# Performance work log

Measured on AMD Instinct MI355X. Metric: run time of the kernel, lower is better.

The kernel has to match this reference:

```python
import jax, jax.numpy as jnp
import numpy as np

B, C, HD, NL, NP = 2, 256, 8, 4, 4
D = C // HD
SHAPES = np.array([[128, 128], [64, 64], [32, 32], [16, 16]], dtype=np.int64)
LV = int(SHAPES.prod(axis=1).sum())  # 21760
LQ = LV


def _bilinear(v_l, loc, Hl, Wl):
    # v_l: [B, HD, Nl, D]; loc: [B, Q, HD, P, 2] normalized to [0,1]
    # Matches torch grid_sample(bilinear, padding='zeros', align_corners=False)
    Bq, Q, _, P, _ = loc.shape
    x = loc[..., 0] * Wl - 0.5
    y = loc[..., 1] * Hl - 0.5
    x0f = jnp.floor(x)
    y0f = jnp.floor(y)
    lx, ly = x - x0f, y - y0f
    x0 = x0f.astype(jnp.int32)
    y0 = y0f.astype(jnp.int32)

    def corner(xi, yi, w):
        valid = (xi >= 0) & (xi < Wl) & (yi >= 0) & (yi < Hl)
        idx = jnp.clip(yi, 0, Hl - 1) * Wl + jnp.clip(xi, 0, Wl - 1)  # [B,Q,HD,P]
        idx = idx.transpose(0, 2, 1, 3).reshape(Bq, HD, Q * P)
        g = jnp.take_along_axis(v_l, idx[..., None], axis=2).reshape(Bq, HD, Q, P, D)
        wm = jnp.where(valid, w, 0.0).transpose(0, 2, 1, 3)[..., None]  # [B,HD,Q,P,1]
        return g * wm

    return (corner(x0, y0, (1 - lx) * (1 - ly))
            + corner(x0 + 1, y0, lx * (1 - ly))
            + corner(x0, y0 + 1, (1 - lx) * ly)
            + corner(x0 + 1, y0 + 1, lx * ly))


def _msda(query, reference_points, value, shapes, W_off, b_off, W_attn, b_attn, W_val, b_val, W_out, b_out):
    # value projection -> per-head layout [B, HD, Lv, D]
    v = (value @ W_val + b_val).reshape(B, LV, HD, D).transpose(0, 2, 1, 3)
    off = (query @ W_off + b_off).reshape(B, LQ, HD, NL, NP, 2)
    aw = jax.nn.softmax((query @ W_attn + b_attn).reshape(B, LQ, HD, NL * NP), axis=-1)
    aw = aw.reshape(B, LQ, HD, NL, NP)
    norm = jnp.asarray(shapes[:, ::-1].copy(), query.dtype)  # (W_l, H_l) per level
    # sampling locations: [B, Lq, HD, NL, NP, 2]
    loc = reference_points[:, :, None, :, None, :] + off / norm[None, None, None, :, None, :]
    out = jnp.zeros((B, HD, LQ, D), query.dtype)
    start = 0
    for l in range(NL):  # small static loop over feature levels
        Hl, Wl = int(shapes[l, 0]), int(shapes[l, 1])
        samp = _bilinear(v[:, :, start:start + Hl * Wl], loc[:, :, :, l], Hl, Wl)  # [B,HD,Q,P,D]
        out = out + jnp.einsum('bhqpd,bhqp->bhqd', samp, aw[:, :, :, l].transpose(0, 2, 1, 3))
        start += Hl * Wl
    out = out.transpose(0, 2, 1, 3).reshape(B, LQ, C)
    # output projection + residual (identity = query, dropout inactive at eval)
    return out @ W_out + b_out + query


def setup_inputs():
    key = jax.random.key(0)
    ks = jax.random.split(key, 8)
    sc = 1.0 / np.sqrt(C)
    return {
        "query": jax.random.normal(ks[0], (B, LQ, C), jnp.float32),
        "reference_points": jax.random.uniform(ks[1], (B, LQ, NL, 2), dtype=jnp.float32),
        "value": jax.random.normal(ks[2], (B, LV, C), jnp.float32),
        "spatial_shapes": SHAPES,
        "level_start_index": np.concatenate([[0], np.cumsum(SHAPES.prod(axis=1))[:-1]]).astype(np.int64),
        "W_off": jax.random.normal(ks[3], (C, HD * NL * NP * 2), jnp.float32) * 0.01,
        "b_off": jax.random.normal(ks[4], (HD * NL * NP * 2,), jnp.float32) * 0.01,
        "W_attn": jax.random.normal(ks[5], (C, HD * NL * NP), jnp.float32) * 0.02,
        "b_attn": jnp.zeros((HD * NL * NP,), jnp.float32),
        "W_val": jax.random.normal(ks[6], (C, C), jnp.float32) * sc,
        "b_val": jnp.zeros((C,), jnp.float32),
        "W_out": jax.random.normal(ks[7], (C, C), jnp.float32) * sc,
        "b_out": jnp.zeros((C,), jnp.float32),
    }


def reference(query, reference_points, value, spatial_shapes, level_start_index, W_off, b_off, W_attn, b_attn, W_val, b_val, W_out, b_out):
    shapes = np.asarray(spatial_shapes)  # static level geometry
    del level_start_index  # level offsets derived directly from shapes
    return _msda(query, reference_points, value, shapes, W_off, b_off, W_attn, b_attn, W_val, b_val, W_out, b_out)
```

## Files before the change

### kernel.cpp

```cpp
#include <hip/hip_runtime.h>

#define LQN 21760
#define LVN 21760
#define BATCH 2
#define CDIM 256
#define HDN 8
#define DDIM 32
#define PADCELLS 22736

typedef __attribute__((ext_vector_type(8))) short short8;
typedef __attribute__((ext_vector_type(4))) float f32x4;
typedef __attribute__((ext_vector_type(2))) float f32x2;

__device__ __forceinline__ unsigned short f2bf(float f) {
  union { float f; unsigned int u; } v; v.f = f;
  unsigned int r = v.u + 0x7fffu + ((v.u >> 16) & 1u);
  return (unsigned short)(r >> 16);
}
__device__ __forceinline__ float bflo(unsigned int u) {
  union { unsigned int u; float f; } v; v.u = u << 16; return v.f;
}
__device__ __forceinline__ float bfhi(unsigned int u) {
  union { unsigned int u; float f; } v; v.u = u & 0xffff0000u; return v.f;
}
__device__ __forceinline__ unsigned pk2bf(float lo, float hi) {
  unsigned r;
  asm("v_cvt_pk_bf16_f32 %0, %1, %2" : "=v"(r) : "v"(lo), "v"(hi));
  return r;
}

template <int IMM>
__device__ __forceinline__ float swzf(float v) {
  return __int_as_float(__builtin_amdgcn_ds_swizzle(__float_as_int(v), IMM));
}
template <int IMM>
__device__ __forceinline__ unsigned swzu(unsigned v) {
  return (unsigned)__builtin_amdgcn_ds_swizzle((int)v, IMM);
}

__global__ __launch_bounds__(256) void prep_zero_kernel(
    const float* __restrict__ Wval, const float* __restrict__ Woff,
    const float* __restrict__ Wattn, const float* __restrict__ Wout,
    unsigned short* __restrict__ wtval, unsigned short* __restrict__ wtoa,
    unsigned short* __restrict__ wtout, unsigned short* __restrict__ vbf) {
  const int b = blockIdx.x;
  if (b < 384) {
    const int idx = b * 256 + threadIdx.x;
    const int n = idx >> 8, k = idx & 255;
    if (idx < 65536) {
      wtval[idx] = f2bf(Wval[k * 256 + n]);
      wtout[idx] = f2bf(Wout[k * 256 + n]);
    }
    const float v = (n < 256) ? Woff[k * 256 + n] : Wattn[k * 128 + (n - 256)];
    wtoa[idx] = f2bf(v);
  } else {
    const int b2 = b - 384;
    const int img = b2 >> 4;
    const int tid = (b2 & 15) * 256 + threadIdx.x;
    const int cell = tid >> 2;
    const int chunk = tid & 3;
    if (cell >= 976) return;
    const int lvl = (cell >= 516) + (cell >= 776) + (cell >= 908);
    const int base = (lvl == 0) ? 0 : (lvl == 1) ? 516 : (lvl == 2) ? 776 : 908;
    const int W2 = (lvl == 0) ? 130 : (lvl == 1) ? 66 : (lvl == 2) ? 34 : 18;
    const int pst = (lvl == 0) ? 0 : (lvl == 1) ? 16900 : (lvl == 2) ? 21256 : 22412;
    const int bb = cell - base;
    int x, y;
    if (bb < W2) { y = 0; x = bb; }
    else if (bb < 2 * W2) { y = W2 - 1; x = bb - W2; }
    else { const int r = bb - 2 * W2; y = 1 + (r >> 1); x = (r & 1) ? (W2 - 1) : 0; }
    const size_t off = (((size_t)img * PADCELLS + pst + y * W2 + x) << 5) + chunk * 8;
    *(uint4*)(vbf + off) = (uint4){0u, 0u, 0u, 0u};
  }
}

template <int MODE>
__device__ __forceinline__ void gemm_body(
    unsigned short* lsA0, unsigned short* lsB0, const int bx, const int by,
    const float* __restrict__ Af32, const unsigned short* __restrict__ Abf,
    const unsigned short* __restrict__ Wt, const float* __restrict__ bias0,
    const float* __restrict__ bias1, const float* __restrict__ resid,
    unsigned short* __restrict__ out_bf, float* __restrict__ out_f32) {
  constexpr int K = 256;
  constexpr int LDSS = 40;
  constexpr int LBUF = 128 * LDSS;
  const int m0 = bx * 128;
  const int n0 = by * 128;
  const int t = threadIdx.x;
  const int w = t >> 6;
  const int l = t & 63;
  const int wr = (w >> 1) * 64;
  const int wc = (w & 1) * 64;
  const int fr = l & 15;
  const int kk = (l >> 4) * 8;

  f32x4 acc[4][4];
#pragma unroll
  for (int mi = 0; mi < 4; ++mi)
#pragma unroll
    for (int ci = 0; ci < 4; ++ci) acc[mi][ci] = (f32x4){0.f, 0.f, 0.f, 0.f};

  const int ar8 = t >> 3, ak8 = (t & 7) * 4;
  const int ar4 = t >> 2, ak4 = (t & 3) * 8;

  float4 fa[4];
  uint4 ua2[2];
  uint4 ub[2];

#define LOADA(kt)                                                            \
  do {                                                                       \
    const int k0_ = (kt) * 32;                                               \
    if (MODE == 2) {                                                         \
      ua2[0] = *(const uint4*)(Abf + (size_t)(m0 + ar4) * K + k0_ + ak4);    \
      ua2[1] = *(const uint4*)(Abf + (size_t)(m0 + 64 + ar4) * K + k0_ + ak4);\
    } else {                                                                 \
      fa[0] = *(const float4*)(Af32 + (size_t)(m0 + ar8) * K + k0_ + ak8);   \
      fa[1] = *(const float4*)(Af32 + (size_t)(m0 + 32 + ar8) * K + k0_ + ak8);\
      fa[2] = *(const float4*)(Af32 + (size_t)(m0 + 64 + ar8) * K + k0_ + ak8);\
      fa[3] = *(const float4*)(Af32 + (size_t)(m0 + 96 + ar8) * K + k0_ + ak8);\
    }                                                                        \
    ub[0] = *(const uint4*)(Wt + (size_t)(n0 + ar4) * K + k0_ + ak4);        \
    ub[1] = *(const uint4*)(Wt + (size_t)(n0 + 64 + ar4) * K + k0_ + ak4);   \
  } while (0)

#define STOREL(buf)                                                          \
  do {                                                                       \
    unsigned short* la = lsA0 + (buf)*LBUF;                                  \
    unsigned short* lb = lsB0 + (buf)*LBUF;                                  \
    if (MODE == 2) {                                                         \
      *(uint4*)(la + ar4 * LDSS + ak4) = ua2[0];                             \
      *(uint4*)(la + (64 + ar4) * LDSS + ak4) = ua2[1];                      \
    } else {                                                                 \
      uint2 q;                                                               \
      q.x = pk2bf(fa[0].x, fa[0].y); q.y = pk2bf(fa[0].z, fa[0].w);          \
      *(uint2*)(la + ar8 * LDSS + ak8) = q;                                  \
      q.x = pk2bf(fa[1].x, fa[1].y); q.y = pk2bf(fa[1].z, fa[1].w);          \
      *(uint2*)(la + (32 + ar8) * LDSS + ak8) = q;                           \
      q.x = pk2bf(fa[2].x, fa[2].y); q.y = pk2bf(fa[2].z, fa[2].w);          \
      *(uint2*)(la + (64 + ar8) * LDSS + ak8) = q;                           \
      q.x = pk2bf(fa[3].x, fa[3].y); q.y = pk2bf(fa[3].z, fa[3].w);          \
      *(uint2*)(la + (96 + ar8) * LDSS + ak8) = q;                           \
    }                                                                        \
    *(uint4*)(lb + ar4 * LDSS + ak4) = ub[0];                                \
    *(uint4*)(lb + (64 + ar4) * LDSS + ak4) = ub[1];                         \
  } while (0)

  LOADA(0);
  STOREL(0);
  __syncthreads();

#pragma unroll
  for (int kt = 0; kt < 8; ++kt) {
    if (kt < 7) LOADA(kt + 1);
    const unsigned short* la = lsA0 + (kt & 1) * LBUF;
    const unsigned short* lb = lsB0 + (kt & 1) * LBUF;
    short8 af[4], bfr[4];
#pragma unroll
    for (int mi = 0; mi < 4; ++mi)
      af[mi] = *(const short8*)(la + (wr + mi * 16 + fr) * LDSS + kk);
#pragma unroll
    for (int ci = 0; ci < 4; ++ci)
      bfr[ci] = *(const short8*)(lb + (wc + ci * 16 + fr) * LDSS + kk);
#pragma unroll
    for (int mi = 0; mi < 4; ++mi)
#pragma unroll
      for (int ci = 0; ci < 4; ++ci)
        acc[mi][ci] = __builtin_amdgcn_mfma_f32_16x16x32_bf16(
            af[mi], bfr[ci], acc[mi][ci], 0, 0, 0);
    if (kt < 7) STOREL((kt + 1) & 1);
    __syncthreads();
  }
#undef LOADA
#undef STOREL

  const int fq = l >> 4;
  if (MODE == 0) {
    int rbase[16];
#pragma unroll
    for (int mi = 0; mi < 4; ++mi) {
#pragma unroll
      for (int r = 0; r < 4; ++r) {
        const int row = m0 + wr + mi * 16 + fq * 4 + r;
        const int bb = (row >= LVN) ? 1 : 0;
        const int i = row - bb * LVN;
        const int lvl = (i >= 16384) + (i >= 20480) + (i >= 21504);
        const int stl = (lvl == 0) ? 0 : (lvl == 1) ? 16384 : (lvl == 2) ? 20480 : 21504;
        const int pst = (lvl == 0) ? 0 : (lvl == 1) ? 16900 : (lvl == 2) ? 21256 : 22412;
        const int lw = 7 - lvl;
        const int Wl = 128 >> lvl;
        const int loc = i - stl;
        const int y = loc >> lw;
        const int x = loc & (Wl - 1);
        const int pidx = pst + (y + 1) * (Wl + 2) + (x + 1);
        rbase[mi * 4 + r] = bb * (HDN * PADCELLS * DDIM) + pidx * DDIM;
      }
    }
#pragma unroll
    for (int ci = 0; ci < 4; ++ci) {
      const int col = n0 + wc + ci * 16 + fr;
      const float bias = bias0[col];
      const int cterm = (col >> 5) * (PADCELLS * DDIM) + (col & 31);
#pragma unroll
      for (int mi = 0; mi < 4; ++mi) {
#pragma unroll
        for (int r = 0; r < 4; r += 2) {
          const unsigned u =
              pk2bf(acc[mi][ci][r] + bias, acc[mi][ci][r + 1] + bias);
          out_bf[(size_t)(rbase[mi * 4 + r] + cterm)] = (unsigned short)u;
          out_bf[(size_t)(rbase[mi * 4 + r + 1] + cterm)] =
              (unsigned short)(u >> 16);
        }
      }
    }
  } else if (MODE == 1) {
#pragma unroll
    for (int ci = 0; ci < 4; ++ci) {
      const int col = n0 + wc + ci * 16 + fr;
      const float bias = (col < 256) ? bias0[col] : bias1[col - 256];
#pragma unroll
      for (int mi = 0; mi < 4; ++mi) {
        const int row0 = m0 + wr + mi * 16 + fq * 4;
#pragma unroll
        for (int r = 0; r < 4; r += 2) {
          const unsigned u =
              pk2bf(acc[mi][ci][r] + bias, acc[mi][ci][r + 1] + bias);
          out_bf[(size_t)(row0 + r) * 384 + col] = (unsigned short)u;
          out_bf[(size_t)(row0 + r + 1) * 384 + col] = (unsigned short)(u >> 16);
        }
      }
    }
  } else {
#pragma unroll
    for (int ci = 0; ci < 4; ++ci) {
      const int col = n0 + wc + ci * 16 + fr;
      const float bias = bias0[col];
#pragma unroll
      for (int mi = 0; mi < 4; ++mi) {
#pragma unroll
        for (int r = 0; r < 4; ++r) {
          const int row = m0 + wr + mi * 16 + fq * 4 + r;
          const size_t o = (size_t)row * 256 + col;
          out_f32[o] = acc[mi][ci][r] + bias + resid[o];
        }
      }
    }
  }
}

__global__ __launch_bounds__(256) void gemm01_kernel(
    const float* __restrict__ value, const float* __restrict__ query,
    const unsigned short* __restrict__ wtval,
    const unsigned short* __restrict__ wtoa, const float* __restrict__ b_val,
    const float* __restrict__ b_off, const float* __restrict__ b_attn,
    unsigned short* __restrict__ vbf, unsigned short* __restrict__ offattn) {
  __shared__ unsigned short lsA[2 * 128 * 40];
  __shared__ unsigned short lsB[2 * 128 * 40];
  const int bid = blockIdx.x;
  const int g = bid % 5, u = bid / 5;
  if (g < 2) {
    gemm_body<0>(lsA, lsB, u, g, value, nullptr, wtval, b_val, nullptr,
                 nullptr, vbf, nullptr);
  } else {
    gemm_body<1>(lsA, lsB, u, g - 2, query, nullptr, wtoa, b_off, b_attn,
                 nullptr, offattn, nullptr);
  }
}

__global__ __launch_bounds__(256) void gemm2_kernel(
    const unsigned short* __restrict__ msout,
    const unsigned short* __restrict__ wtout, const float* __restrict__ b_out,
    const float* __restrict__ query, float* __restrict__ out) {
  __shared__ unsigned short lsA[2 * 128 * 40];
  __shared__ unsigned short lsB[2 * 128 * 40];
  gemm_body<2>(lsA, lsB, blockIdx.x, blockIdx.y, nullptr, msout, wtout, b_out,
               nullptr, query, nullptr, out);
}

__global__ __launch_bounds__(256) void sampler_kernel(
    const unsigned short* __restrict__ vbf,
    const unsigned short* __restrict__ offattn,
    const float* __restrict__ refpts,
    unsigned short* __restrict__ msout) {
  const int lid = blockIdx.x;
  const int pair = lid & 7;
  const int k = lid >> 3;
  const int img = pair * 2 + (k & 1);
  const int qchunk = k >> 1;
  const int h = img & 7;
  const int bb = img >> 3;

  const int t = threadIdx.x;
  const int lane = t & 63;
  const int qloc = qchunk * 64 + (t >> 6) * 16 + (lane >> 2);
  const int qi = bb * LQN + qloc;
  const int j = lane & 3;
  const int d0 = j * 8;

  const unsigned short* oa = offattn + (size_t)qi * 384;

  const int Wl = 128 >> j;
  const int W2 = Wl + 2;
  const int pst = (j == 0) ? 0 : (j == 1) ? 16900 : (j == 2) ? 21256 : 22412;
  const float fw = (float)Wl;

  const uint2 lr = *(const uint2*)(oa + 256 + h * 16 + j * 4);
  const float l0 = bflo(lr.x), l1 = bfhi(lr.x);
  const float l2 = bflo(lr.y), l3 = bfhi(lr.y);
  float mx = fmaxf(fmaxf(l0, l1), fmaxf(l2, l3));
  mx = fmaxf(mx, swzf<0x041F>(mx));
  mx = fmaxf(mx, swzf<0x081F>(mx));
  const float e0v = __expf(l0 - mx), e1v = __expf(l1 - mx);
  const float e2v = __expf(l2 - mx), e3v = __expf(l3 - mx);
  float s = (e0v + e1v) + (e2v + e3v);
  s += swzf<0x041F>(s);
  s += swzf<0x081F>(s);
  const float inv = 1.f / s;
  const float aw4[4] = {e0v * inv, e1v * inv, e2v * inv, e3v * inv};

  const float2 rf = *(const float2*)(refpts + (size_t)qi * 8 + j * 2);
  const uint4 ov = *(const uint4*)(oa + h * 32 + j * 8);
  const unsigned op_[4] = {ov.x, ov.y, ov.z, ov.w};

  unsigned eo[4][4];
  float wt[4][4];
#pragma unroll
  for (int pt = 0; pt < 4; ++pt) {
    const float ox = bflo(op_[pt]);
    const float oy = bfhi(op_[pt]);
    const float xs = fmaf(rf.x, fw, ox) - 0.5f;
    const float ys = fmaf(rf.y, fw, oy) - 0.5f;
    const float x0f = floorf(xs), y0f = floorf(ys);
    const float lx = xs - x0f, ly = ys - y0f;
    const int x0 = (int)x0f, y0 = (int)y0f;
    const float a = aw4[pt];
    const float wy1 = a * ly, wy0 = a - wy1;
    const float w01v = wy0 * lx, w00v = wy0 - w01v;
    const float w11v = wy1 * lx, w10v = wy1 - w11v;
    const int xb0 = min(max(x0 + 1, 0), Wl + 1);
    const int xb1 = min(max(x0 + 2, 0), Wl + 1);
    const int yb0 = min(max(y0 + 1, 0), Wl + 1);
    const int yb1 = min(max(y0 + 2, 0), Wl + 1);
    const unsigned r0 = (unsigned)(pst + yb0 * W2);
    const unsigned r1 = (unsigned)(pst + yb1 * W2);
    eo[pt][0] = (r0 + xb0) << 5;
    eo[pt][1] = (r0 + xb1) << 5;
    eo[pt][2] = (r1 + xb0) << 5;
    eo[pt][3] = (r1 + xb1) << 5;
    wt[pt][0] = w00v; wt[pt][1] = w01v; wt[pt][2] = w10v; wt[pt][3] = w11v;
  }

  const unsigned headbase =
      (unsigned)img * (PADCELLS * DDIM) + (unsigned)d0;

  f32x2 acc0 = (f32x2){0.f, 0.f}, acc1 = (f32x2){0.f, 0.f};
  f32x2 acc2 = (f32x2){0.f, 0.f}, acc3 = (f32x2){0.f, 0.f};

#define ACCUM(rv, wgt)                                 \
  {                                                    \
    f32x2 v_;                                          \
    v_.x = bflo(rv.x); v_.y = bfhi(rv.x);              \
    acc0 += v_ * (wgt);                                \
    v_.x = bflo(rv.y); v_.y = bfhi(rv.y);              \
    acc1 += v_ * (wgt);                                \
    v_.x = bflo(rv.z); v_.y = bfhi(rv.z);              \
    acc2 += v_ * (wgt);                                \
    v_.x = bflo(rv.w); v_.y = bfhi(rv.w);              \
    acc3 += v_ * (wgt);                                \
  }

#define POINT(LVL, PT)                                                  \
  {                                                                     \
    constexpr int IMM = (LVL << 5) | 0x1C;                              \
    const unsigned o00 = swzu<IMM>(eo[PT][0]);                          \
    const unsigned o01 = swzu<IMM>(eo[PT][1]);                          \
    const unsigned o10 = swzu<IMM>(eo[PT][2]);                          \
    const unsigned o11 = swzu<IMM>(eo[PT][3]);                          \
    const float w00 = swzf<IMM>(wt[PT][0]);                             \
    const float w01 = swzf<IMM>(wt[PT][1]);                             \
    const float w10 = swzf<IMM>(wt[PT][2]);                             \
    const float w11 = swzf<IMM>(wt[PT][3]);                             \
    const uint4 v00 = *(const uint4*)(vbf + headbase + o00);            \
    const uint4 v01 = *(const uint4*)(vbf + headbase + o01);            \
    const uint4 v10 = *(const uint4*)(vbf + headbase + o10);            \
    const uint4 v11 = *(const uint4*)(vbf + headbase + o11);            \
    ACCUM(v00, w00)                                                     \
    ACCUM(v01, w01)                                                     \
    ACCUM(v10, w10)                                                     \
    ACCUM(v11, w11)                                                     \
  }

  POINT(0, 0) POINT(0, 1) POINT(0, 2) POINT(0, 3)
  POINT(1, 0) POINT(1, 1) POINT(1, 2) POINT(1, 3)
  POINT(2, 0) POINT(2, 1) POINT(2, 2) POINT(2, 3)
  POINT(3, 0) POINT(3, 1) POINT(3, 2) POINT(3, 3)
#undef POINT
#undef ACCUM

  uint4 outv;
  outv.x = pk2bf(acc0.x, acc0.y);
  outv.y = pk2bf(acc1.x, acc1.y);
  outv.z = pk2bf(acc2.x, acc2.y);
  outv.w = pk2bf(acc3.x, acc3.y);
  *(uint4*)(msout + (size_t)qi * 256 + h * 32 + d0) = outv;
}

extern "C" void kernel_launch(void* const* d_in, const int* in_sizes, int n_in,
                              void* d_out, int out_size, void* d_ws,
                              size_t ws_size, hipStream_t stream) {
  const float* query = (const float*)d_in[0];
  const float* refpts = (const float*)d_in[1];
  const float* value = (const float*)d_in[2];
  const float* W_off = (const float*)d_in[5];
  const float* b_off = (const float*)d_in[6];
  const float* W_attn = (const float*)d_in[7];
  const float* b_attn = (const float*)d_in[8];
  const float* W_val = (const float*)d_in[9];
  const float* b_val = (const float*)d_in[10];
  const float* W_out = (const float*)d_in[11];
  const float* b_out = (const float*)d_in[12];
  float* out = (float*)d_out;

  char* ws = (char*)d_ws;
  unsigned short* wtval = (unsigned short*)(ws);
  unsigned short* wtoa = (unsigned short*)(ws + 131072);
  unsigned short* wtout = (unsigned short*)(ws + 327680);
  unsigned short* vbf = (unsigned short*)(ws + 458752);
  unsigned short* offattn = (unsigned short*)(ws + 23740416);
  unsigned short* msout = (unsigned short*)(ws + 57163776);

  prep_zero_kernel<<<640, 256, 0, stream>>>(W_val, W_off, W_attn, W_out, wtval,
                                            wtoa, wtout, vbf);
  gemm01_kernel<<<1700, 256, 0, stream>>>(value, query, wtval, wtoa, b_val,
                                          b_off, b_attn, vbf, offattn);
  sampler_kernel<<<5440, 256, 0, stream>>>(vbf, offattn, refpts, msout);
  gemm2_kernel<<<dim3(340, 2), 256, 0, stream>>>(msout, wtout, b_out, query,
                                                 out);
}
```

Measured before the change: 165.4 us.

## Process two queries per sampler thread and remap GEMM block order for XCD locality

The sampler now handles two queries per thread, 64 apart, and interleaves their bilinear gathers. This halves the grid and gives each thread more independent loads in flight to hide gather latency. Both GEMM kernels get a new block-index remap that groups 8 consecutive M-tiles across the column tiles, so blocks sharing A or B tiles land on the same XCD under round-robin dispatch. The grids are padded and surplus blocks exit early. The cost is higher register pressure in the sampler, which may reduce occupancy.

```diff
diff --git a/kernel.cpp b/kernel.cpp
--- a/kernel.cpp
+++ b/kernel.cpp
@@ -253,10 +253,15 @@
     const unsigned short* __restrict__ wtoa, const float* __restrict__ b_val,
     const float* __restrict__ b_off, const float* __restrict__ b_attn,
     unsigned short* __restrict__ vbf, unsigned short* __restrict__ offattn) {
+  const int bid = blockIdx.x;
+  const int q = bid / 40;
+  const int rem = bid % 40;
+  const int g = rem >> 3;
+  const int r = rem & 7;
+  const int u = q * 8 + r;
+  if (u >= 340) return;
   __shared__ unsigned short lsA[2 * 128 * 40];
   __shared__ unsigned short lsB[2 * 128 * 40];
-  const int bid = blockIdx.x;
-  const int g = bid % 5, u = bid / 5;
   if (g < 2) {
     gemm_body<0>(lsA, lsB, u, g, value, nullptr, wtval, b_val, nullptr,
                  nullptr, vbf, nullptr);
@@ -270,10 +275,17 @@
     const unsigned short* __restrict__ msout,
     const unsigned short* __restrict__ wtout, const float* __restrict__ b_out,
     const float* __restrict__ query, float* __restrict__ out) {
+  const int bid = blockIdx.x;
+  const int q = bid / 16;
+  const int rem = bid % 16;
+  const int y = rem >> 3;
+  const int r = rem & 7;
+  const int u = q * 8 + r;
+  if (u >= 340) return;
   __shared__ unsigned short lsA[2 * 128 * 40];
   __shared__ unsigned short lsB[2 * 128 * 40];
-  gemm_body<2>(lsA, lsB, blockIdx.x, blockIdx.y, nullptr, msout, wtout, b_out,
-               nullptr, query, nullptr, out);
+  gemm_body<2>(lsA, lsB, u, y, nullptr, msout, wtout, b_out, nullptr, query,
+               nullptr, out);
 }
 
 __global__ __launch_bounds__(256) void sampler_kernel(
@@ -291,117 +303,137 @@
 
   const int t = threadIdx.x;
   const int lane = t & 63;
-  const int qloc = qchunk * 64 + (t >> 6) * 16 + (lane >> 2);
-  const int qi = bb * LQN + qloc;
+  const int wv = t >> 6;
   const int j = lane & 3;
   const int d0 = j * 8;
-
-  const unsigned short* oa = offattn + (size_t)qi * 384;
+  const int q0 = qchunk * 128 + wv * 16 + (lane >> 2);
+  const int qi0 = bb * LQN + q0;
+  const int qi1 = qi0 + 64;
+
+  const unsigned short* oa0 = offattn + (size_t)qi0 * 384;
+  const unsigned short* oa1 = offattn + (size_t)qi1 * 384;
 
   const int Wl = 128 >> j;
   const int W2 = Wl + 2;
   const int pst = (j == 0) ? 0 : (j == 1) ? 16900 : (j == 2) ? 21256 : 22412;
   const float fw = (float)Wl;
 
-  const uint2 lr = *(const uint2*)(oa + 256 + h * 16 + j * 4);
-  const float l0 = bflo(lr.x), l1 = bfhi(lr.x);
-  const float l2 = bflo(lr.y), l3 = bfhi(lr.y);
-  float mx = fmaxf(fmaxf(l0, l1), fmaxf(l2, l3));
-  mx = fmaxf(mx, swzf<0x041F>(mx));
-  mx = fmaxf(mx, swzf<0x081F>(mx));
-  const float e0v = __expf(l0 - mx), e1v = __expf(l1 - mx);
-  const float e2v = __expf(l2 - mx), e3v = __expf(l3 - mx);
-  float s = (e0v + e1v) + (e2v + e3v);
-  s += swzf<0x041F>(s);
-  s += swzf<0x081F>(s);
-  const float inv = 1.f / s;
-  const float aw4[4] = {e0v * inv, e1v * inv, e2v * inv, e3v * inv};
-
-  const float2 rf = *(const float2*)(refpts + (size_t)qi * 8 + j * 2);
-  const uint4 ov = *(const uint4*)(oa + h * 32 + j * 8);
-  const unsigned op_[4] = {ov.x, ov.y, ov.z, ov.w};
-
-  unsigned eo[4][4];
-  float wt[4][4];
+  float aw0[4], aw1[4];
+#define SOFTMAX(OA, AW)                                        \
+  {                                                            \
+    const uint2 lr = *(const uint2*)((OA) + 256 + h * 16 + j * 4); \
+    const float l0 = bflo(lr.x), l1 = bfhi(lr.x);              \
+    const float l2 = bflo(lr.y), l3 = bfhi(lr.y);              \
+    float mx = fmaxf(fmaxf(l0, l1), fmaxf(l2, l3));            \
+    mx = fmaxf(mx, swzf<0x041F>(mx));                          \
+    mx = fmaxf(mx, swzf<0x081F>(mx));                          \
+    const float e0 = __expf(l0 - mx), e1 = __expf(l1 - mx);    \
+    const float e2 = __expf(l2 - mx), e3 = __expf(l3 - mx);    \
+    float s = (e0 + e1) + (e2 + e3);                           \
+    s += swzf<0x041F>(s);                                      \
+    s += swzf<0x081F>(s);                                      \
+    const float inv = 1.f / s;                                 \
+    AW[0] = e0 * inv; AW[1] = e1 * inv;                        \
+    AW[2] = e2 * inv; AW[3] = e3 * inv;                        \
+  }
+  SOFTMAX(oa0, aw0)
+  SOFTMAX(oa1, aw1)
+#undef SOFTMAX
+
+  const float2 rf0 = *(const float2*)(refpts + (size_t)qi0 * 8 + j * 2);
+  const float2 rf1 = *(const float2*)(refpts + (size_t)qi1 * 8 + j * 2);
+  const uint4 ov0 = *(const uint4*)(oa0 + h * 32 + j * 8);
+  const uint4 ov1 = *(const uint4*)(oa1 + h * 32 + j * 8);
+  const unsigned op0_[4] = {ov0.x, ov0.y, ov0.z, ov0.w};
+  const unsigned op1_[4] = {ov1.x, ov1.y, ov1.z, ov1.w};
+
+  const unsigned short* vb =
+      vbf + (size_t)img * (PADCELLS * DDIM) + d0;
+
+  f32x2 ac0[4], ac1[4];
+#pragma unroll
+  for (int c = 0; c < 4; ++c) {
+    ac0[c] = (f32x2){0.f, 0.f};
+    ac1[c] = (f32x2){0.f, 0.f};
+  }
+
+#define OWNER(OPW, RF, AWV, EO, WT)                      \
+  {                                                      \
+    const float ox = bflo(OPW), oy = bfhi(OPW);          \
+    const float xs = fmaf((RF).x, fw, ox) - 0.5f;        \
+    const float ys = fmaf((RF).y, fw, oy) - 0.5f;        \
+    const float x0f = floorf(xs), y0f = floorf(ys);      \
+    const float lx = xs - x0f, ly = ys - y0f;            \
+    const int x0 = (int)x0f, y0 = (int)y0f;              \
+    const float wy1 = (AWV)*ly, wy0 = (AWV)-wy1;         \
+    WT[1] = wy0 * lx; WT[0] = wy0 - WT[1];               \
+    WT[3] = wy1 * lx; WT[2] = wy1 - WT[3];               \
+    const int xb0 = min(max(x0 + 1, 0), Wl + 1);         \
+    const int xb1 = min(max(x0 + 2, 0), Wl + 1);         \
+    const int yb0 = min(max(y0 + 1, 0), Wl + 1);         \
+    const int yb1 = min(max(y0 + 2, 0), Wl + 1);         \
+    const unsigned r0 = (unsigned)(pst + yb0 * W2);      \
+    const unsigned r1 = (unsigned)(pst + yb1 * W2);      \
+    EO[0] = (r0 + xb0) << 5; EO[1] = (r0 + xb1) << 5;    \
+    EO[2] = (r1 + xb0) << 5; EO[3] = (r1 + xb1) << 5;    \
+  }
+
+#define ACC4(AC, rv, wgt)                                \
+  {                                                      \
+    f32x2 v_;                                            \
+    v_.x = bflo(rv.x); v_.y = bfhi(rv.x); AC[0] += v_ * (wgt); \
+    v_.x = bflo(rv.y); v_.y = bfhi(rv.y); AC[1] += v_ * (wgt); \
+    v_.x = bflo(rv.z); v_.y = bfhi(rv.z); AC[2] += v_ * (wgt); \
+    v_.x = bflo(rv.w); v_.y = bfhi(rv.w); AC[3] += v_ * (wgt); \
+  }
+
+#define PL(LVL, EO, WT, AC)                              \
+  {                                                      \
+    constexpr int IMM = ((LVL) << 5) | 0x1C;             \
+    const unsigned o00 = swzu<IMM>(EO[0]);               \
+    const unsigned o01 = swzu<IMM>(EO[1]);               \
+    const unsigned o10 = swzu<IMM>(EO[2]);               \
+    const unsigned o11 = swzu<IMM>(EO[3]);               \
+    const float w00 = swzf<IMM>(WT[0]);                  \
+    const float w01 = swzf<IMM>(WT[1]);                  \
+    const float w10 = swzf<IMM>(WT[2]);                  \
+    const float w11 = swzf<IMM>(WT[3]);                  \
+    const uint4 v00 = *(const uint4*)(vb + o00);         \
+    const uint4 v01 = *(const uint4*)(vb + o01);         \
+    const uint4 v10 = *(const uint4*)(vb + o10);         \
+    const uint4 v11 = *(const uint4*)(vb + o11);         \
+    ACC4(AC, v00, w00)                                   \
+    ACC4(AC, v01, w01)                                   \
+    ACC4(AC, v10, w10)                                   \
+    ACC4(AC, v11, w11)                                   \
+  }
+
 #pragma unroll
   for (int pt = 0; pt < 4; ++pt) {
-    const float ox = bflo(op_[pt]);
-    const float oy = bfhi(op_[pt]);
-    const float xs = fmaf(rf.x, fw, ox) - 0.5f;
-    const float ys = fmaf(rf.y, fw, oy) - 0.5f;
-    const float x0f = floorf(xs), y0f = floorf(ys);
-    const float lx = xs - x0f, ly = ys - y0f;
-    const int x0 = (int)x0f, y0 = (int)y0f;
-    const float a = aw4[pt];
-    const float wy1 = a * ly, wy0 = a - wy1;
-    const float w01v = wy0 * lx, w00v = wy0 - w01v;
-    const float w11v = wy1 * lx, w10v = wy1 - w11v;
-    const int xb0 = min(max(x0 + 1, 0), Wl + 1);
-    const int xb1 = min(max(x0 + 2, 0), Wl + 1);
-    const int yb0 = min(max(y0 + 1, 0), Wl + 1);
-    const int yb1 = min(max(y0 + 2, 0), Wl + 1);
-    const unsigned r0 = (unsigned)(pst + yb0 * W2);
-    const unsigned r1 = (unsigned)(pst + yb1 * W2);
-    eo[pt][0] = (r0 + xb0) << 5;
-    eo[pt][1] = (r0 + xb1) << 5;
-    eo[pt][2] = (r1 + xb0) << 5;
-    eo[pt][3] = (r1 + xb1) << 5;
-    wt[pt][0] = w00v; wt[pt][1] = w01v; wt[pt][2] = w10v; wt[pt][3] = w11v;
-  }
-
-  const unsigned headbase =
-      (unsigned)img * (PADCELLS * DDIM) + (unsigned)d0;
-
-  f32x2 acc0 = (f32x2){0.f, 0.f}, acc1 = (f32x2){0.f, 0.f};
-  f32x2 acc2 = (f32x2){0.f, 0.f}, acc3 = (f32x2){0.f, 0.f};
-
-#define ACCUM(rv, wgt)                                 \
-  {                                                    \
-    f32x2 v_;                                          \
-    v_.x = bflo(rv.x); v_.y = bfhi(rv.x);              \
-    acc0 += v_ * (wgt);                                \
-    v_.x = bflo(rv.y); v_.y = bfhi(rv.y);              \
-    acc1 += v_ * (wgt);                                \
-    v_.x = bflo(rv.z); v_.y = bfhi(rv.z);              \
-    acc2 += v_ * (wgt);                                \
-    v_.x = bflo(rv.w); v_.y = bfhi(rv.w);              \
-    acc3 += v_ * (wgt);                                \
-  }
-
-#define POINT(LVL, PT)                                                  \
-  {                                                                     \
-    constexpr int IMM = (LVL << 5) | 0x1C;                              \
-    const unsigned o00 = swzu<IMM>(eo[PT][0]);                          \
-    const unsigned o01 = swzu<IMM>(eo[PT][1]);                          \
-    const unsigned o10 = swzu<IMM>(eo[PT][2]);                          \
-    const unsigned o11 = swzu<IMM>(eo[PT][3]);                          \
-    const float w00 = swzf<IMM>(wt[PT][0]);                             \
-    const float w01 = swzf<IMM>(wt[PT][1]);                             \
-    const float w10 = swzf<IMM>(wt[PT][2]);                             \
-    const float w11 = swzf<IMM>(wt[PT][3]);                             \
-    const uint4 v00 = *(const uint4*)(vbf + headbase + o00);            \
-    const uint4 v01 = *(const uint4*)(vbf + headbase + o01);            \
-    const uint4 v10 = *(const uint4*)(vbf + headbase + o10);            \
-    const uint4 v11 = *(const uint4*)(vbf + headbase + o11);            \
-    ACCUM(v00, w00)                                                     \
-    ACCUM(v01, w01)                                                     \
-    ACCUM(v10, w10)                                                     \
-    ACCUM(v11, w11)                                                     \
-  }
-
-  POINT(0, 0) POINT(0, 1) POINT(0, 2) POINT(0, 3)
-  POINT(1, 0) POINT(1, 1) POINT(1, 2) POINT(1, 3)
-  POINT(2, 0) POINT(2, 1) POINT(2, 2) POINT(2, 3)
-  POINT(3, 0) POINT(3, 1) POINT(3, 2) POINT(3, 3)
-#undef POINT
-#undef ACCUM
-
-  uint4 outv;
-  outv.x = pk2bf(acc0.x, acc0.y);
-  outv.y = pk2bf(acc1.x, acc1.y);
-  outv.z = pk2bf(acc2.x, acc2.y);
-  outv.w = pk2bf(acc3.x, acc3.y);
-  *(uint4*)(msout + (size_t)qi * 256 + h * 32 + d0) = outv;
+    unsigned eo0[4], eo1[4];
+    float wt0[4], wt1[4];
+    OWNER(op0_[pt], rf0, aw0[pt], eo0, wt0)
+    OWNER(op1_[pt], rf1, aw1[pt], eo1, wt1)
+    PL(0, eo0, wt0, ac0) PL(0, eo1, wt1, ac1)
+    PL(1, eo0, wt0, ac0) PL(1, eo1, wt1, ac1)
+    PL(2, eo0, wt0, ac0) PL(2, eo1, wt1, ac1)
+    PL(3, eo0, wt0, ac0) PL(3, eo1, wt1, ac1)
+  }
+#undef PL
+#undef ACC4
+#undef OWNER
+
+  uint4 o0, o1;
+  o0.x = pk2bf(ac0[0].x, ac0[0].y);
+  o0.y = pk2bf(ac0[1].x, ac0[1].y);
+  o0.z = pk2bf(ac0[2].x, ac0[2].y);
+  o0.w = pk2bf(ac0[3].x, ac0[3].y);
+  o1.x = pk2bf(ac1[0].x, ac1[0].y);
+  o1.y = pk2bf(ac1[1].x, ac1[1].y);
+  o1.z = pk2bf(ac1[2].x, ac1[2].y);
+  o1.w = pk2bf(ac1[3].x, ac1[3].y);
+  *(uint4*)(msout + (size_t)qi0 * 256 + h * 32 + d0) = o0;
+  *(uint4*)(msout + (size_t)qi1 * 256 + h * 32 + d0) = o1;
 }
 
 extern "C" void kernel_launch(void* const* d_in, const int* in_sizes, int n_in,
@@ -430,9 +462,8 @@
 
   prep_zero_kernel<<<640, 256, 0, stream>>>(W_val, W_off, W_attn, W_out, wtval,
                                             wtoa, wtout, vbf);
-  gemm01_kernel<<<1700, 256, 0, stream>>>(value, query, wtval, wtoa, b_val,
+  gemm01_kernel<<<1720, 256, 0, stream>>>(value, query, wtval, wtoa, b_val,
                                           b_off, b_attn, vbf, offattn);
-  sampler_kernel<<<5440, 256, 0, stream>>>(vbf, offattn, refpts, msout);
-  gemm2_kernel<<<dim3(340, 2), 256, 0, stream>>>(msout, wtout, b_out, query,
-                                                 out);
-}
+  sampler_kernel<<<2720, 256, 0, stream>>>(vbf, offattn, refpts, msout);
+  gemm2_kernel<<<688, 256, 0, stream>>>(msout, wtout, b_out, query, out);
+}
```

Result: faster. 151.0 us (-8.7%).
